# Kernel tuning notes

Measured on AMD Instinct MI355X. Metric: run time of the kernel, lower is better.

Reference implementation:

```python
import jax, jax.numpy as jnp
import numpy as np
import math

D_MODEL = 1024
N_HEADS = 16
SEQ = 2048
BATCH = 2


def setup_inputs() -> dict:
    key = jax.random.key(0)
    ks = jax.random.split(key, 7)
    scale = 1.0 / math.sqrt(D_MODEL)
    return {
        "q": jax.random.normal(ks[0], (SEQ, BATCH, D_MODEL), jnp.float32),
        "k": jax.random.normal(ks[1], (SEQ, BATCH, D_MODEL), jnp.float32),
        "v": jax.random.normal(ks[2], (SEQ, BATCH, D_MODEL), jnp.float32),
        "in_proj_w": jax.random.normal(ks[3], (3 * D_MODEL, D_MODEL), jnp.float32) * scale,
        "in_proj_b": jax.random.normal(ks[4], (3 * D_MODEL,), jnp.float32) * 0.01,
        "out_proj_w": jax.random.normal(ks[5], (D_MODEL, D_MODEL), jnp.float32) * scale,
        "out_proj_b": jax.random.normal(ks[6], (D_MODEL,), jnp.float32) * 0.01,
    }


def reference(q, k, v, in_proj_w, in_proj_b, out_proj_w, out_proj_b):
    # q, k, v: (S, B, D) seq-first layout as in the torch module
    S, B, D = q.shape
    H = N_HEADS
    dk = D // H
    wq, wk, wv = jnp.split(in_proj_w, 3, axis=0)   # each (D, D)
    bq, bk, bv = jnp.split(in_proj_b, 3, axis=0)   # each (D,)
    qp = q @ wq.T + bq
    kp = k @ wk.T + bk
    vp = v @ wv.T + bv
    # (S, B, D) -> (S, B*H, dk) -> (B*H, S, dk)
    def to_heads(x, s):
        return x.reshape(s, B * H, dk).transpose(1, 0, 2)
    qh = to_heads(qp, S)
    kh = to_heads(kp, k.shape[0])
    vh = to_heads(vp, v.shape[0])
    # scores: (B*H, Sq, Sk)
    scores = jnp.einsum('bqd,bkd->bqk', qh, kh) / math.sqrt(dk)
    probs = jax.nn.softmax(scores, axis=-1)
    attn = jnp.einsum('bqk,bkd->bqd', probs, vh)   # (B*H, S, dk)
    # (B*H, S, dk) -> (S, B*H, dk) -> (S*B, D)
    attn = attn.transpose(1, 0, 2).reshape(S * B, D)
    out = attn @ out_proj_w.T + out_proj_b
    return out.reshape(S, B, D)
```

## Files before the change

kernel.cpp:

```cpp
#include <hip/hip_runtime.h>
#include <math.h>

#define SEQ    2048
#define BATCH  2
#define DMODEL 1024
#define NHEADS 16
#define DK     64

typedef __attribute__((ext_vector_type(8))) short  bf16x8;
typedef __attribute__((ext_vector_type(4))) float  f32x4;
typedef __attribute__((ext_vector_type(8))) unsigned short u16x8;

#define GLD16(gp, lp) __builtin_amdgcn_global_load_lds(                      \
    (__attribute__((address_space(1))) void*)(gp),                            \
    (__attribute__((address_space(3))) void*)(lp), 16, 0, 0)

__device__ inline unsigned short f2bf(float f) {
    unsigned int u = __float_as_uint(f);
    u += 0x7fffu + ((u >> 16) & 1u);
    return (unsigned short)(u >> 16);
}

__device__ inline unsigned int pk2bf(float a, float b) {
#if __has_builtin(__builtin_amdgcn_cvt_pk_bf16_f32)
    typedef __attribute__((ext_vector_type(2))) __bf16 v2bf;
    v2bf r = __builtin_amdgcn_cvt_pk_bf16_f32(a, b);
    unsigned int u; __builtin_memcpy(&u, &r, 4); return u;
#else
    return (unsigned int)f2bf(a) | ((unsigned int)f2bf(b) << 16);
#endif
}

__device__ inline float fast_exp2(float x) {
#if __has_builtin(__builtin_amdgcn_exp2f)
    return __builtin_amdgcn_exp2f(x);
#else
    return __expf(x * 0.69314718055994531f);
#endif
}

#define WS_QB   0u
#define WS_KB   4194304u
#define WS_VB   8388608u
#define WS_WIB  12582912u
#define WS_WOB  15728640u
#define WS_QH   16777216u
#define WS_KH   20971520u
#define WS_VT   25165824u
#define WS_ATT  29360128u

__global__ __launch_bounds__(256) void cast_all_kernel(
    const float* __restrict__ q, const float* __restrict__ k,
    const float* __restrict__ v, const float* __restrict__ w_in,
    const float* __restrict__ w_out, unsigned short* __restrict__ ws)
{
    const int gid = blockIdx.x * 256 + threadIdx.x;
    const float* src; unsigned short* dst;
    if (gid < 524288)       { int g = gid;           src = q     + (size_t)g*8; dst = ws + WS_QB  + (size_t)g*8; }
    else if (gid < 1048576) { int g = gid - 524288;  src = k     + (size_t)g*8; dst = ws + WS_KB  + (size_t)g*8; }
    else if (gid < 1572864) { int g = gid - 1048576; src = v     + (size_t)g*8; dst = ws + WS_VB  + (size_t)g*8; }
    else if (gid < 1966080) { int g = gid - 1572864; src = w_in  + (size_t)g*8; dst = ws + WS_WIB + (size_t)g*8; }
    else                    { int g = gid - 1966080; src = w_out + (size_t)g*8; dst = ws + WS_WOB + (size_t)g*8; }
    float4 a = *(const float4*)src;
    float4 b = *(const float4*)(src + 4);
    u16x8 o;
    o[0]=f2bf(a.x); o[1]=f2bf(a.y); o[2]=f2bf(a.z); o[3]=f2bf(a.w);
    o[4]=f2bf(b.x); o[5]=f2bf(b.y); o[6]=f2bf(b.z); o[7]=f2bf(b.w);
    *(u16x8*)dst = o;
}

__global__ __launch_bounds__(256) void qkv_gemm_kernel(
    const unsigned short* __restrict__ ws_in, const float* __restrict__ bias,
    unsigned short* __restrict__ ws_out)
{
    __shared__ unsigned short As[128*32];
    __shared__ unsigned short Bs[128*32];

    const int t    = threadIdx.x;
    const int lane = t & 63;
    const int w    = t >> 6;
    const int lrow = lane & 15;
    const int quad = lane >> 4;
    const int wm   = (w >> 1) * 64;
    const int wn   = (w & 1) * 64;

    const int n0    = blockIdx.x * 128;
    const int m0    = blockIdx.y * 128;
    const int which = n0 >> 10;

    const unsigned short* A = ws_in + WS_QB + (size_t)which * 4194304u;
    const unsigned short* B = ws_in + WS_WIB;

    const int srow = t >> 2;
    const int scc  = (t & 3) ^ ((t >> 3) & 3);
    const unsigned short* gA0 = A + (size_t)(m0 + srow) * 1024 + scc * 8;
    const unsigned short* gA1 = A + (size_t)(m0 + 64 + srow) * 1024 + scc * 8;
    const unsigned short* gB0 = B + (size_t)(n0 + srow) * 1024 + scc * 8;
    const unsigned short* gB1 = B + (size_t)(n0 + 64 + srow) * 1024 + scc * 8;

    f32x4 acc[4][4] = {};

    #pragma unroll 1
    for (int kt = 0; kt < 1024; kt += 32) {
        __syncthreads();
        GLD16(gA0, As + (size_t)t * 8);
        GLD16(gA1, As + (size_t)(t + 256) * 8);
        GLD16(gB0, Bs + (size_t)t * 8);
        GLD16(gB1, Bs + (size_t)(t + 256) * 8);
        gA0 += 32; gA1 += 32; gB0 += 32; gB1 += 32;
        __syncthreads();

        bf16x8 af[4], bf[4];
        #pragma unroll
        for (int mt = 0; mt < 4; ++mt) {
            const int r = wm + mt*16 + lrow;
            af[mt] = *(const bf16x8*)(As + r*32 + ((quad ^ ((r>>1)&3))*8));
        }
        #pragma unroll
        for (int nt = 0; nt < 4; ++nt) {
            const int r = wn + nt*16 + lrow;
            bf[nt] = *(const bf16x8*)(Bs + r*32 + ((quad ^ ((r>>1)&3))*8));
        }
        #pragma unroll
        for (int mt = 0; mt < 4; ++mt)
            #pragma unroll
            for (int nt = 0; nt < 4; ++nt)
                acc[mt][nt] = __builtin_amdgcn_mfma_f32_16x16x32_bf16(
                    af[mt], bf[nt], acc[mt][nt], 0, 0, 0);
    }

    unsigned short* dstQK = ws_out + WS_QH + (size_t)which * 4194304u;
    unsigned short* dstV  = ws_out + WS_VT;
    const float qscale = 0.18033688011112042f;

    #pragma unroll
    for (int nt = 0; nt < 4; ++nt) {
        const int n = n0 + wn + nt*16 + lrow;
        const float bn = bias[n];
        const int h = (n & 1023) >> 6;
        const int d = n & 63;
        #pragma unroll
        for (int mt = 0; mt < 4; ++mt) {
            if (which < 2) {
                #pragma unroll
                for (int r = 0; r < 4; ++r) {
                    const int m = m0 + wm + mt*16 + quad*4 + r;
                    const int s = m >> 1, b = m & 1;
                    float val = acc[mt][nt][r] + bn;
                    if (which == 0) val *= qscale;
                    dstQK[((size_t)((b<<4) + h) * 2048 + s) * 64 + d] = f2bf(val);
                }
            } else {
                const int m_base = m0 + wm + mt*16 + quad*4;
                const int s0 = m_base >> 1;
                unsigned int pk0 = pk2bf(acc[mt][nt][0] + bn, acc[mt][nt][2] + bn);
                unsigned int pk1 = pk2bf(acc[mt][nt][1] + bn, acc[mt][nt][3] + bn);
                *(unsigned int*)(dstV + ((size_t)h*64 + d)*2048 + s0)        = pk0;
                *(unsigned int*)(dstV + ((size_t)(16 + h)*64 + d)*2048 + s0) = pk1;
            }
        }
    }
}

__global__ __launch_bounds__(256) void attn_mfma_kernel(
    const unsigned short* __restrict__ qh, const unsigned short* __restrict__ kh,
    const unsigned short* __restrict__ vt, unsigned short* __restrict__ attn)
{
    __shared__ unsigned short Qs[64*64];
    __shared__ unsigned short Ks[64*64];
    __shared__ unsigned short Vts[80*64];
    __shared__ unsigned short Ps[64*64];

    const int t    = threadIdx.x;
    const int lane = t & 63;
    const int w    = t >> 6;
    const int lrow = lane & 15;
    const int quad = lane >> 4;

    const int qt = blockIdx.x;
    const int bh = blockIdx.y;

    const unsigned short* Qg = qh + ((size_t)bh * 2048 + qt * 64) * 64;
    const unsigned short* Kb = kh + (size_t)bh * 2048 * 64;
    const unsigned short* Vb = vt + (size_t)bh * 64 * 2048;

    #pragma unroll
    for (int i = 0; i < 2; ++i) {
        const int c = i*256 + t;
        const int row = c >> 3, cc = (c & 7) ^ (row & 7);
        GLD16(Qg + (size_t)row*64 + cc*8, Qs + (size_t)c*8);
    }
    if (t < 128) {
        const int row = 64 + (t >> 3);
        const unsigned short fill = (row == 64) ? (unsigned short)0x3F80 : (unsigned short)0;
        u16x8 cv;
        #pragma unroll
        for (int j = 0; j < 8; ++j) cv[j] = fill;
        *(u16x8*)(Vts + row*64 + (t & 7)*8) = cv;
    }

    f32x4 O[5] = {};
    float m_i = -INFINITY;

    #pragma unroll 1
    for (int ktile = 0; ktile < 32; ++ktile) {
        __syncthreads();
        const unsigned short* Kg = Kb + (size_t)ktile * 64 * 64;
        const unsigned short* Vg = Vb + (size_t)ktile * 64;
        #pragma unroll
        for (int i = 0; i < 2; ++i) {
            const int c = i*256 + t;
            const int row = c >> 3, cc = (c & 7) ^ (row & 7);
            GLD16(Kg + (size_t)row*64   + cc*8, Ks  + (size_t)c*8);
            GLD16(Vg + (size_t)row*2048 + cc*8, Vts + (size_t)c*8);
        }
        __syncthreads();

        f32x4 ST[4] = {};
        #pragma unroll
        for (int kk = 0; kk < 2; ++kk) {
            const int qr = w*16 + lrow;
            bf16x8 qf = *(const bf16x8*)(Qs + qr*64 + (((kk*4+quad) ^ (qr&7))*8));
            #pragma unroll
            for (int m = 0; m < 4; ++m) {
                const int r = m*16 + lrow;
                bf16x8 kf = *(const bf16x8*)(Ks + r*64 + (((kk*4+quad) ^ (r&7))*8));
                ST[m] = __builtin_amdgcn_mfma_f32_16x16x32_bf16(kf, qf, ST[m], 0, 0, 0);
            }
        }

        float mm = fmaxf(fmaxf(ST[0][0], ST[0][1]), fmaxf(ST[0][2], ST[0][3]));
        #pragma unroll
        for (int m = 1; m < 4; ++m)
            mm = fmaxf(mm, fmaxf(fmaxf(ST[m][0], ST[m][1]),
                                 fmaxf(ST[m][2], ST[m][3])));
        mm = fmaxf(mm, __shfl_xor(mm, 16, 64));
        mm = fmaxf(mm, __shfl_xor(mm, 32, 64));

        if (__any(mm > m_i)) {
            const float mn = fmaxf(m_i, mm);
            const float al = fast_exp2(m_i - mn);
            m_i = mn;
            #pragma unroll
            for (int d = 0; d < 5; ++d) O[d] *= al;
        }

        const int prow = w*16 + lrow;
        #pragma unroll
        for (int m = 0; m < 4; ++m) {
            const float p0 = fast_exp2(ST[m][0] - m_i);
            const float p1 = fast_exp2(ST[m][1] - m_i);
            const float p2 = fast_exp2(ST[m][2] - m_i);
            const float p3 = fast_exp2(ST[m][3] - m_i);
            uint2 pk;
            pk.x = pk2bf(p0, p1);
            pk.y = pk2bf(p2, p3);
            const int sc = (m*2 + (quad >> 1)) ^ (prow & 7);
            *(uint2*)(Ps + prow*64 + sc*8 + (quad & 1)*4) = pk;
        }

        #pragma unroll
        for (int kk = 0; kk < 2; ++kk) {
            bf16x8 pf = *(const bf16x8*)(Ps + prow*64 + (((kk*4+quad) ^ (prow&7))*8));
            #pragma unroll
            for (int d = 0; d < 5; ++d) {
                const int r = d*16 + lrow;
                bf16x8 vf = *(const bf16x8*)(Vts + r*64 + (((kk*4+quad) ^ (r&7))*8));
                O[d] = __builtin_amdgcn_mfma_f32_16x16x32_bf16(vf, pf, O[d], 0, 0, 0);
            }
        }
    }

    const float lv = O[4][0];
    const float l  = __shfl(lv, lrow, 64);
    const float inv = 1.f / l;

    const int b_ = bh >> 4, h_ = bh & 15;
    const int s_ = qt*64 + w*16 + lrow;
    unsigned short* dst = attn + ((size_t)(s_*2 + b_)) * 1024 + h_*64;
    #pragma unroll
    for (int dt = 0; dt < 4; ++dt) {
        uint2 pk;
        pk.x = pk2bf(O[dt][0]*inv, O[dt][1]*inv);
        pk.y = pk2bf(O[dt][2]*inv, O[dt][3]*inv);
        *(uint2*)(dst + dt*16 + quad*4) = pk;
    }
}

__global__ __launch_bounds__(256) void out_gemm_kernel(
    const unsigned short* __restrict__ A, const unsigned short* __restrict__ B,
    const float* __restrict__ bias, float* __restrict__ out)
{
    __shared__ unsigned short As[64*32];
    __shared__ unsigned short Bs[128*32];

    const int t    = threadIdx.x;
    const int lane = t & 63;
    const int w    = t >> 6;
    const int lrow = lane & 15;
    const int quad = lane >> 4;
    const int wn   = (w >> 1) * 64;
    const int wm   = (w & 1) * 32;

    const int n0 = blockIdx.x * 128;
    const int m0 = blockIdx.y * 64;

    const int srow = t >> 2;
    const int scc  = (t & 3) ^ ((t >> 3) & 3);
    const unsigned short* gA0 = A + (size_t)(m0 + srow) * 1024 + scc * 8;
    const unsigned short* gB0 = B + (size_t)(n0 + srow) * 1024 + scc * 8;
    const unsigned short* gB1 = B + (size_t)(n0 + 64 + srow) * 1024 + scc * 8;

    f32x4 acc[2][4] = {};

    #pragma unroll 1
    for (int kt = 0; kt < 1024; kt += 32) {
        __syncthreads();
        GLD16(gA0, As + (size_t)t * 8);
        GLD16(gB0, Bs + (size_t)t * 8);
        GLD16(gB1, Bs + (size_t)(t + 256) * 8);
        gA0 += 32; gB0 += 32; gB1 += 32;
        __syncthreads();

        bf16x8 af[2], bf[4];
        #pragma unroll
        for (int mt = 0; mt < 2; ++mt) {
            const int r = wm + mt*16 + lrow;
            af[mt] = *(const bf16x8*)(As + r*32 + ((quad ^ ((r>>1)&3))*8));
        }
        #pragma unroll
        for (int nt = 0; nt < 4; ++nt) {
            const int r = wn + nt*16 + lrow;
            bf[nt] = *(const bf16x8*)(Bs + r*32 + ((quad ^ ((r>>1)&3))*8));
        }
        #pragma unroll
        for (int mt = 0; mt < 2; ++mt)
            #pragma unroll
            for (int nt = 0; nt < 4; ++nt)
                acc[mt][nt] = __builtin_amdgcn_mfma_f32_16x16x32_bf16(
                    af[mt], bf[nt], acc[mt][nt], 0, 0, 0);
    }

    #pragma unroll
    for (int nt = 0; nt < 4; ++nt) {
        const int n = n0 + wn + nt*16 + lrow;
        const float bn = bias[n];
        #pragma unroll
        for (int mt = 0; mt < 2; ++mt) {
            #pragma unroll
            for (int r = 0; r < 4; ++r) {
                const int m = m0 + wm + mt*16 + quad*4 + r;
                out[(size_t)m * 1024 + n] = acc[mt][nt][r] + bn;
            }
        }
    }
}

extern "C" void kernel_launch(void* const* d_in, const int* in_sizes, int n_in,
                              void* d_out, int out_size, void* d_ws, size_t ws_size,
                              hipStream_t stream) {
    const float* q     = (const float*)d_in[0];
    const float* k     = (const float*)d_in[1];
    const float* v     = (const float*)d_in[2];
    const float* w_in  = (const float*)d_in[3];
    const float* b_in  = (const float*)d_in[4];
    const float* w_out = (const float*)d_in[5];
    const float* b_out = (const float*)d_in[6];
    float* out = (float*)d_out;

    unsigned short* ws = (unsigned short*)d_ws;

    cast_all_kernel<<<8192, 256, 0, stream>>>(q, k, v, w_in, w_out, ws);
    qkv_gemm_kernel<<<dim3(24, 32), 256, 0, stream>>>(ws, b_in, ws);
    attn_mfma_kernel<<<dim3(32, 32), 256, 0, stream>>>(
        ws + WS_QH, ws + WS_KH, ws + WS_VT, ws + WS_ATT);
    out_gemm_kernel<<<dim3(8, 64), 256, 0, stream>>>(
        ws + WS_ATT, ws + WS_WOB, b_out, out);
}
```

Measured before the change: 252.5 us.

## Store Q/K projections row-major with vectorized epilogues and strided attention loads

The QKV projection swaps the MFMA operand order for Q and K, so each lane holds four consecutive output columns. Those results are written as packed 8-byte stores into a row-major (S*B, D) layout instead of scattered 2-byte stores into a head-major layout. The attention kernel now reads Q and K tiles with a 2048-element row stride from that layout. The output GEMM also swaps operands so it can write float4 stores with a float4 bias load. This aims to cut uncoalesced scalar global stores, at the cost of strided 128-byte row loads in attention.

Measured after the change: 265.2 us. 1.05x slower.

```diff
diff --git a/kernel.cpp b/kernel.cpp
--- a/kernel.cpp
+++ b/kernel.cpp
@@ -121,36 +121,53 @@
             const int r = wn + nt*16 + lrow;
             bf[nt] = *(const bf16x8*)(Bs + r*32 + ((quad ^ ((r>>1)&3))*8));
         }
-        #pragma unroll
-        for (int mt = 0; mt < 4; ++mt)
-            #pragma unroll
-            for (int nt = 0; nt < 4; ++nt)
-                acc[mt][nt] = __builtin_amdgcn_mfma_f32_16x16x32_bf16(
-                    af[mt], bf[nt], acc[mt][nt], 0, 0, 0);
-    }
-
-    unsigned short* dstQK = ws_out + WS_QH + (size_t)which * 4194304u;
-    unsigned short* dstV  = ws_out + WS_VT;
-    const float qscale = 0.18033688011112042f;
-
-    #pragma unroll
-    for (int nt = 0; nt < 4; ++nt) {
-        const int n = n0 + wn + nt*16 + lrow;
-        const float bn = bias[n];
-        const int h = (n & 1023) >> 6;
-        const int d = n & 63;
-        #pragma unroll
-        for (int mt = 0; mt < 4; ++mt) {
-            if (which < 2) {
+        if (which < 2) {
+            #pragma unroll
+            for (int mt = 0; mt < 4; ++mt)
                 #pragma unroll
-                for (int r = 0; r < 4; ++r) {
-                    const int m = m0 + wm + mt*16 + quad*4 + r;
-                    const int s = m >> 1, b = m & 1;
-                    float val = acc[mt][nt][r] + bn;
-                    if (which == 0) val *= qscale;
-                    dstQK[((size_t)((b<<4) + h) * 2048 + s) * 64 + d] = f2bf(val);
-                }
-            } else {
+                for (int nt = 0; nt < 4; ++nt)
+                    acc[mt][nt] = __builtin_amdgcn_mfma_f32_16x16x32_bf16(
+                        bf[nt], af[mt], acc[mt][nt], 0, 0, 0);
+        } else {
+            #pragma unroll
+            for (int mt = 0; mt < 4; ++mt)
+                #pragma unroll
+                for (int nt = 0; nt < 4; ++nt)
+                    acc[mt][nt] = __builtin_amdgcn_mfma_f32_16x16x32_bf16(
+                        af[mt], bf[nt], acc[mt][nt], 0, 0, 0);
+        }
+    }
+
+    if (which < 2) {
+        unsigned short* dst = ws_out + WS_QH + (size_t)which * 4194304u;
+        const float qs = (which == 0) ? 0.18033688011112042f : 1.0f;
+        #pragma unroll
+        for (int nt = 0; nt < 4; ++nt) {
+            const int n = n0 + wn + nt*16 + quad*4;
+            const float4 b4 = *(const float4*)(bias + n);
+            #pragma unroll
+            for (int mt = 0; mt < 4; ++mt) {
+                const int m = m0 + wm + mt*16 + lrow;
+                const float v0 = (acc[mt][nt][0] + b4.x) * qs;
+                const float v1 = (acc[mt][nt][1] + b4.y) * qs;
+                const float v2 = (acc[mt][nt][2] + b4.z) * qs;
+                const float v3 = (acc[mt][nt][3] + b4.w) * qs;
+                uint2 pk;
+                pk.x = pk2bf(v0, v1);
+                pk.y = pk2bf(v2, v3);
+                *(uint2*)(dst + (size_t)m*1024 + (n & 1023)) = pk;
+            }
+        }
+    } else {
+        unsigned short* dstV = ws_out + WS_VT;
+        #pragma unroll
+        for (int nt = 0; nt < 4; ++nt) {
+            const int n = n0 + wn + nt*16 + lrow;
+            const float bn = bias[n];
+            const int h = (n & 1023) >> 6;
+            const int d = n & 63;
+            #pragma unroll
+            for (int mt = 0; mt < 4; ++mt) {
                 const int m_base = m0 + wm + mt*16 + quad*4;
                 const int s0 = m_base >> 1;
                 unsigned int pk0 = pk2bf(acc[mt][nt][0] + bn, acc[mt][nt][2] + bn);
@@ -179,16 +196,17 @@
 
     const int qt = blockIdx.x;
     const int bh = blockIdx.y;
-
-    const unsigned short* Qg = qh + ((size_t)bh * 2048 + qt * 64) * 64;
-    const unsigned short* Kb = kh + (size_t)bh * 2048 * 64;
+    const int b_ = bh >> 4, h_ = bh & 15;
+
+    const unsigned short* Qg = qh + (size_t)(qt*128 + b_)*1024 + h_*64;
+    const unsigned short* Kb = kh;
     const unsigned short* Vb = vt + (size_t)bh * 64 * 2048;
 
     #pragma unroll
     for (int i = 0; i < 2; ++i) {
         const int c = i*256 + t;
         const int row = c >> 3, cc = (c & 7) ^ (row & 7);
-        GLD16(Qg + (size_t)row*64 + cc*8, Qs + (size_t)c*8);
+        GLD16(Qg + (size_t)row*2048 + cc*8, Qs + (size_t)c*8);
     }
     if (t < 128) {
         const int row = 64 + (t >> 3);
@@ -205,13 +223,13 @@
     #pragma unroll 1
     for (int ktile = 0; ktile < 32; ++ktile) {
         __syncthreads();
-        const unsigned short* Kg = Kb + (size_t)ktile * 64 * 64;
+        const unsigned short* Kg = Kb + (size_t)(ktile*128 + b_)*1024 + h_*64;
         const unsigned short* Vg = Vb + (size_t)ktile * 64;
         #pragma unroll
         for (int i = 0; i < 2; ++i) {
             const int c = i*256 + t;
             const int row = c >> 3, cc = (c & 7) ^ (row & 7);
-            GLD16(Kg + (size_t)row*64   + cc*8, Ks  + (size_t)c*8);
+            GLD16(Kg + (size_t)row*2048 + cc*8, Ks  + (size_t)c*8);
             GLD16(Vg + (size_t)row*2048 + cc*8, Vts + (size_t)c*8);
         }
         __syncthreads();
@@ -275,7 +293,6 @@
     const float l  = __shfl(lv, lrow, 64);
     const float inv = 1.f / l;
 
-    const int b_ = bh >> 4, h_ = bh & 15;
     const int s_ = qt*64 + w*16 + lrow;
     unsigned short* dst = attn + ((size_t)(s_*2 + b_)) * 1024 + h_*64;
     #pragma unroll
@@ -338,20 +355,22 @@
             #pragma unroll
             for (int nt = 0; nt < 4; ++nt)
                 acc[mt][nt] = __builtin_amdgcn_mfma_f32_16x16x32_bf16(
-                    af[mt], bf[nt], acc[mt][nt], 0, 0, 0);
+                    bf[nt], af[mt], acc[mt][nt], 0, 0, 0);
     }
 
     #pragma unroll
     for (int nt = 0; nt < 4; ++nt) {
-        const int n = n0 + wn + nt*16 + lrow;
-        const float bn = bias[n];
+        const int n = n0 + wn + nt*16 + quad*4;
+        const float4 b4 = *(const float4*)(bias + n);
         #pragma unroll
         for (int mt = 0; mt < 2; ++mt) {
-            #pragma unroll
-            for (int r = 0; r < 4; ++r) {
-                const int m = m0 + wm + mt*16 + quad*4 + r;
-                out[(size_t)m * 1024 + n] = acc[mt][nt][r] + bn;
-            }
+            const int m = m0 + wm + mt*16 + lrow;
+            float4 o;
+            o.x = acc[mt][nt][0] + b4.x;
+            o.y = acc[mt][nt][1] + b4.y;
+            o.z = acc[mt][nt][2] + b4.z;
+            o.w = acc[mt][nt][3] + b4.w;
+            *(float4*)(out + (size_t)m*1024 + n) = o;
         }
     }
 }
```

## Fuse fp32-to-bf16 casting into GEMM tile loads and drop cast kernel

Applied to the files above, without the earlier changes.

Removes the standalone cast kernel. The QKV and output-projection GEMMs now read fp32 inputs and weights directly from global memory, pack them to bf16 in registers and store them into swizzled LDS. This saves a kernel launch and a full write and reread of the bf16 copies. In exchange each GEMM block re-reads and re-converts fp32 tiles, which doubles the global bytes per tile and adds conversion ALU work. It also gives up the async global_load_lds path for those operands, and loads are still not double-buffered.

Result: slower. 284.4 us (+12.6%).

```diff
diff --git a/kernel.cpp b/kernel.cpp
--- a/kernel.cpp
+++ b/kernel.cpp
@@ -31,6 +31,15 @@
 #endif
 }
 
+__device__ inline u16x8 pk8bf(float4 a, float4 b) {
+    union { u16x8 v; unsigned int u[4]; } r;
+    r.u[0] = pk2bf(a.x, a.y);
+    r.u[1] = pk2bf(a.z, a.w);
+    r.u[2] = pk2bf(b.x, b.y);
+    r.u[3] = pk2bf(b.z, b.w);
+    return r.v;
+}
+
 __device__ inline float fast_exp2(float x) {
 #if __has_builtin(__builtin_amdgcn_exp2f)
     return __builtin_amdgcn_exp2f(x);
@@ -39,39 +48,15 @@
 #endif
 }
 
-#define WS_QB   0u
-#define WS_KB   4194304u
-#define WS_VB   8388608u
-#define WS_WIB  12582912u
-#define WS_WOB  15728640u
-#define WS_QH   16777216u
-#define WS_KH   20971520u
-#define WS_VT   25165824u
-#define WS_ATT  29360128u
-
-__global__ __launch_bounds__(256) void cast_all_kernel(
+#define WS_QH   0u
+#define WS_KH   4194304u
+#define WS_VT   8388608u
+#define WS_ATT  12582912u
+
+__global__ __launch_bounds__(256) void qkv_gemm_kernel(
     const float* __restrict__ q, const float* __restrict__ k,
     const float* __restrict__ v, const float* __restrict__ w_in,
-    const float* __restrict__ w_out, unsigned short* __restrict__ ws)
-{
-    const int gid = blockIdx.x * 256 + threadIdx.x;
-    const float* src; unsigned short* dst;
-    if (gid < 524288)       { int g = gid;           src = q     + (size_t)g*8; dst = ws + WS_QB  + (size_t)g*8; }
-    else if (gid < 1048576) { int g = gid - 524288;  src = k     + (size_t)g*8; dst = ws + WS_KB  + (size_t)g*8; }
-    else if (gid < 1572864) { int g = gid - 1048576; src = v     + (size_t)g*8; dst = ws + WS_VB  + (size_t)g*8; }
-    else if (gid < 1966080) { int g = gid - 1572864; src = w_in  + (size_t)g*8; dst = ws + WS_WIB + (size_t)g*8; }
-    else                    { int g = gid - 1966080; src = w_out + (size_t)g*8; dst = ws + WS_WOB + (size_t)g*8; }
-    float4 a = *(const float4*)src;
-    float4 b = *(const float4*)(src + 4);
-    u16x8 o;
-    o[0]=f2bf(a.x); o[1]=f2bf(a.y); o[2]=f2bf(a.z); o[3]=f2bf(a.w);
-    o[4]=f2bf(b.x); o[5]=f2bf(b.y); o[6]=f2bf(b.z); o[7]=f2bf(b.w);
-    *(u16x8*)dst = o;
-}
-
-__global__ __launch_bounds__(256) void qkv_gemm_kernel(
-    const unsigned short* __restrict__ ws_in, const float* __restrict__ bias,
-    unsigned short* __restrict__ ws_out)
+    const float* __restrict__ bias, unsigned short* __restrict__ ws_out)
 {
     __shared__ unsigned short As[128*32];
     __shared__ unsigned short Bs[128*32];
@@ -88,26 +73,35 @@
     const int m0    = blockIdx.y * 128;
     const int which = n0 >> 10;
 
-    const unsigned short* A = ws_in + WS_QB + (size_t)which * 4194304u;
-    const unsigned short* B = ws_in + WS_WIB;
-
-    const int srow = t >> 2;
-    const int scc  = (t & 3) ^ ((t >> 3) & 3);
-    const unsigned short* gA0 = A + (size_t)(m0 + srow) * 1024 + scc * 8;
-    const unsigned short* gA1 = A + (size_t)(m0 + 64 + srow) * 1024 + scc * 8;
-    const unsigned short* gB0 = B + (size_t)(n0 + srow) * 1024 + scc * 8;
-    const unsigned short* gB1 = B + (size_t)(n0 + 64 + srow) * 1024 + scc * 8;
+    const float* A = (which == 0) ? q : (which == 1) ? k : v;
+    const float* B = w_in;
+
+    const int sr  = t >> 1;
+    const int sh  = (t & 1) * 16;
+    const int swz = (sr >> 1) & 3;
+    const int g0  = (t & 1) * 2;
+    const float* gA = A + (size_t)(m0 + sr) * 1024 + sh;
+    const float* gB = B + (size_t)(n0 + sr) * 1024 + sh;
+    unsigned short* wA = As + sr*32;
+    unsigned short* wB = Bs + sr*32;
 
     f32x4 acc[4][4] = {};
 
     #pragma unroll 1
     for (int kt = 0; kt < 1024; kt += 32) {
-        __syncthreads();
-        GLD16(gA0, As + (size_t)t * 8);
-        GLD16(gA1, As + (size_t)(t + 256) * 8);
-        GLD16(gB0, Bs + (size_t)t * 8);
-        GLD16(gB1, Bs + (size_t)(t + 256) * 8);
-        gA0 += 32; gA1 += 32; gB0 += 32; gB1 += 32;
+        float4 a0 = *(const float4*)(gA + kt);
+        float4 a1 = *(const float4*)(gA + kt + 4);
+        float4 a2 = *(const float4*)(gA + kt + 8);
+        float4 a3 = *(const float4*)(gA + kt + 12);
+        float4 b0 = *(const float4*)(gB + kt);
+        float4 b1 = *(const float4*)(gB + kt + 4);
+        float4 b2 = *(const float4*)(gB + kt + 8);
+        float4 b3 = *(const float4*)(gB + kt + 12);
+        __syncthreads();
+        *(u16x8*)(wA + ((g0     ^ swz) * 8)) = pk8bf(a0, a1);
+        *(u16x8*)(wA + (((g0+1) ^ swz) * 8)) = pk8bf(a2, a3);
+        *(u16x8*)(wB + ((g0     ^ swz) * 8)) = pk8bf(b0, b1);
+        *(u16x8*)(wB + (((g0+1) ^ swz) * 8)) = pk8bf(b2, b3);
         __syncthreads();
 
         bf16x8 af[4], bf[4];
@@ -288,7 +282,7 @@
 }
 
 __global__ __launch_bounds__(256) void out_gemm_kernel(
-    const unsigned short* __restrict__ A, const unsigned short* __restrict__ B,
+    const unsigned short* __restrict__ A, const float* __restrict__ B,
     const float* __restrict__ bias, float* __restrict__ out)
 {
     __shared__ unsigned short As[64*32];
@@ -305,21 +299,29 @@
     const int n0 = blockIdx.x * 128;
     const int m0 = blockIdx.y * 64;
 
-    const int srow = t >> 2;
-    const int scc  = (t & 3) ^ ((t >> 3) & 3);
-    const unsigned short* gA0 = A + (size_t)(m0 + srow) * 1024 + scc * 8;
-    const unsigned short* gB0 = B + (size_t)(n0 + srow) * 1024 + scc * 8;
-    const unsigned short* gB1 = B + (size_t)(n0 + 64 + srow) * 1024 + scc * 8;
+    const int srowA = t >> 2;
+    const int sccA  = (t & 3) ^ ((t >> 3) & 3);
+    const unsigned short* gA0 = A + (size_t)(m0 + srowA) * 1024 + sccA * 8;
+
+    const int sr  = t >> 1;
+    const int sh  = (t & 1) * 16;
+    const int swz = (sr >> 1) & 3;
+    const int g0  = (t & 1) * 2;
+    const float* gB = B + (size_t)(n0 + sr) * 1024 + sh;
+    unsigned short* wB = Bs + sr*32;
 
     f32x4 acc[2][4] = {};
 
     #pragma unroll 1
     for (int kt = 0; kt < 1024; kt += 32) {
-        __syncthreads();
-        GLD16(gA0, As + (size_t)t * 8);
-        GLD16(gB0, Bs + (size_t)t * 8);
-        GLD16(gB1, Bs + (size_t)(t + 256) * 8);
-        gA0 += 32; gB0 += 32; gB1 += 32;
+        float4 b0 = *(const float4*)(gB + kt);
+        float4 b1 = *(const float4*)(gB + kt + 4);
+        float4 b2 = *(const float4*)(gB + kt + 8);
+        float4 b3 = *(const float4*)(gB + kt + 12);
+        __syncthreads();
+        GLD16(gA0 + kt, As + (size_t)t * 8);
+        *(u16x8*)(wB + ((g0     ^ swz) * 8)) = pk8bf(b0, b1);
+        *(u16x8*)(wB + (((g0+1) ^ swz) * 8)) = pk8bf(b2, b3);
         __syncthreads();
 
         bf16x8 af[2], bf[4];
@@ -370,10 +372,9 @@
 
     unsigned short* ws = (unsigned short*)d_ws;
 
-    cast_all_kernel<<<8192, 256, 0, stream>>>(q, k, v, w_in, w_out, ws);
-    qkv_gemm_kernel<<<dim3(24, 32), 256, 0, stream>>>(ws, b_in, ws);
+    qkv_gemm_kernel<<<dim3(24, 32), 256, 0, stream>>>(q, k, v, w_in, b_in, ws);
     attn_mfma_kernel<<<dim3(32, 32), 256, 0, stream>>>(
         ws + WS_QH, ws + WS_KH, ws + WS_VT, ws + WS_ATT);
     out_gemm_kernel<<<dim3(8, 64), 256, 0, stream>>>(
-        ws + WS_ATT, ws + WS_WOB, b_out, out);
-}
+        ws + WS_ATT, w_out, b_out, out);
+}
```

## Double-buffer K/V tiles in attention kernel to overlap loads with compute

Applied to the files above, without the earlier changes.

Doubles the K and V^T shared-memory buffers and issues the asynchronous global-to-LDS load for the next key tile before computing on the current one. The prologue loads tile 0 and fills the constant rows of both V buffers, and one barrier per iteration replaces two. The aim is to hide global load latency behind the MFMA and softmax work. In exchange, LDS use grows by about 18 KB per block, which can lower occupancy. The overlap may also be lost if the compiler places conservative vmcnt waits before the LDS reads.

Measured after the change: 258.7 us. +2.5%, slower.

```diff
diff --git a/kernel.cpp b/kernel.cpp
--- a/kernel.cpp
+++ b/kernel.cpp
@@ -167,8 +167,8 @@
     const unsigned short* __restrict__ vt, unsigned short* __restrict__ attn)
 {
     __shared__ unsigned short Qs[64*64];
-    __shared__ unsigned short Ks[64*64];
-    __shared__ unsigned short Vts[80*64];
+    __shared__ unsigned short Ks[2][64*64];
+    __shared__ unsigned short Vts[2][80*64];
     __shared__ unsigned short Ps[64*64];
 
     const int t    = threadIdx.x;
@@ -190,13 +190,21 @@
         const int row = c >> 3, cc = (c & 7) ^ (row & 7);
         GLD16(Qg + (size_t)row*64 + cc*8, Qs + (size_t)c*8);
     }
+    #pragma unroll
+    for (int i = 0; i < 2; ++i) {
+        const int c = i*256 + t;
+        const int row = c >> 3, cc = (c & 7) ^ (row & 7);
+        GLD16(Kb + (size_t)row*64   + cc*8, Ks[0]  + (size_t)c*8);
+        GLD16(Vb + (size_t)row*2048 + cc*8, Vts[0] + (size_t)c*8);
+    }
     if (t < 128) {
         const int row = 64 + (t >> 3);
         const unsigned short fill = (row == 64) ? (unsigned short)0x3F80 : (unsigned short)0;
         u16x8 cv;
         #pragma unroll
         for (int j = 0; j < 8; ++j) cv[j] = fill;
-        *(u16x8*)(Vts + row*64 + (t & 7)*8) = cv;
+        *(u16x8*)(Vts[0] + row*64 + (t & 7)*8) = cv;
+        *(u16x8*)(Vts[1] + row*64 + (t & 7)*8) = cv;
     }
 
     f32x4 O[5] = {};
@@ -205,16 +213,23 @@
     #pragma unroll 1
     for (int ktile = 0; ktile < 32; ++ktile) {
         __syncthreads();
-        const unsigned short* Kg = Kb + (size_t)ktile * 64 * 64;
-        const unsigned short* Vg = Vb + (size_t)ktile * 64;
-        #pragma unroll
-        for (int i = 0; i < 2; ++i) {
-            const int c = i*256 + t;
-            const int row = c >> 3, cc = (c & 7) ^ (row & 7);
-            GLD16(Kg + (size_t)row*64   + cc*8, Ks  + (size_t)c*8);
-            GLD16(Vg + (size_t)row*2048 + cc*8, Vts + (size_t)c*8);
-        }
-        __syncthreads();
+        const int cur = ktile & 1;
+
+        if (ktile < 31) {
+            const int nxt = cur ^ 1;
+            const unsigned short* Kg = Kb + (size_t)(ktile+1) * 64 * 64;
+            const unsigned short* Vg = Vb + (size_t)(ktile+1) * 64;
+            #pragma unroll
+            for (int i = 0; i < 2; ++i) {
+                const int c = i*256 + t;
+                const int row = c >> 3, cc = (c & 7) ^ (row & 7);
+                GLD16(Kg + (size_t)row*64   + cc*8, Ks[nxt]  + (size_t)c*8);
+                GLD16(Vg + (size_t)row*2048 + cc*8, Vts[nxt] + (size_t)c*8);
+            }
+        }
+
+        const unsigned short* Kcur = Ks[cur];
+        const unsigned short* Vcur = Vts[cur];
 
         f32x4 ST[4] = {};
         #pragma unroll
@@ -224,7 +239,7 @@
             #pragma unroll
             for (int m = 0; m < 4; ++m) {
                 const int r = m*16 + lrow;
-                bf16x8 kf = *(const bf16x8*)(Ks + r*64 + (((kk*4+quad) ^ (r&7))*8));
+                bf16x8 kf = *(const bf16x8*)(Kcur + r*64 + (((kk*4+quad) ^ (r&7))*8));
                 ST[m] = __builtin_amdgcn_mfma_f32_16x16x32_bf16(kf, qf, ST[m], 0, 0, 0);
             }
         }
@@ -265,7 +280,7 @@
             #pragma unroll
             for (int d = 0; d < 5; ++d) {
                 const int r = d*16 + lrow;
-                bf16x8 vf = *(const bf16x8*)(Vts + r*64 + (((kk*4+quad) ^ (r&7))*8));
+                bf16x8 vf = *(const bf16x8*)(Vcur + r*64 + (((kk*4+quad) ^ (r&7))*8));
                 O[d] = __builtin_amdgcn_mfma_f32_16x16x32_bf16(vf, pf, O[d], 0, 0, 0);
             }
         }
```
